# Kernel optimization log

Hardware: AMD Instinct MI355X
Metric: run time of the kernel (lower is better)

The kernel has to match this reference:

```python
import jax, jax.numpy as jnp
import numpy as np

EPS = 1e-5

def cal_pcm(cen, s):
    # circ_shift in the original is exactly a circular roll of the HxW plane.
    r = lambda dy, dx: jnp.roll(cen, (dy, dx), axis=(2, 3))
    s1 = (r(-s, -s) - cen) * (r(s, s) - cen)   # NW/SE diagonal pair
    s2 = (r(-s, 0) - cen) * (r(s, 0) - cen)    # N/S pair
    s3 = (r(-s, s) - cen) * (r(s, -s) - cen)   # NE/SW diagonal pair
    s4 = (r(0, s) - cen) * (r(0, -s) - cen)    # E/W pair
    return jnp.minimum(jnp.minimum(s1, s2), jnp.minimum(s3, s4))

def batchnorm(x, gamma, beta):
    # training-mode BN: batch statistics over (N,H,W)
    mean = x.mean(axis=(0, 2, 3), keepdims=True)
    var = x.var(axis=(0, 2, 3), keepdims=True)
    xn = (x - mean) * jax.lax.rsqrt(var + EPS)
    return xn * gamma[None, :, None, None] + beta[None, :, None, None]

def se_att(x, w1, b1, g1, be1, w2, b2, g2, be2):
    # AdaptiveAvgPool2d(1) -> 1x1 conv -> BN -> ReLU -> 1x1 conv -> BN -> Sigmoid
    p = x.mean(axis=(2, 3), keepdims=True)                      # [B,C,1,1]
    y = jnp.einsum('oc,bcij->boij', w1, p) + b1[None, :, None, None]
    y = jax.nn.relu(batchnorm(y, g1, be1))
    y = jnp.einsum('oc,bcij->boij', w2, y) + b2[None, :, None, None]
    return jax.nn.sigmoid(batchnorm(y, g2, be2))

def setup_inputs() -> dict:
    key = jax.random.key(0)
    ks = jax.random.split(key, 8)
    B, C, H, W = 4, 64, 384, 384
    IC = C // 2
    inp = {
        'cen': jax.random.normal(ks[0], (B, C, H, W), dtype=jnp.float32),
        'bn1_g': jnp.ones((C,), jnp.float32), 'bn1_b': jnp.zeros((C,), jnp.float32),
        'bn2_g': jnp.ones((C,), jnp.float32), 'bn2_b': jnp.zeros((C,), jnp.float32),
        'td_w1': jax.random.normal(ks[1], (IC, C), jnp.float32) * 0.1,
        'td_b1': jnp.zeros((IC,), jnp.float32),
        'td_g1': jnp.ones((IC,), jnp.float32), 'td_be1': jnp.zeros((IC,), jnp.float32),
        'td_w2': jax.random.normal(ks[2], (C, IC), jnp.float32) * 0.1,
        'td_b2': jnp.zeros((C,), jnp.float32),
        'td_g2': jnp.ones((C,), jnp.float32), 'td_be2': jnp.zeros((C,), jnp.float32),
        'bu_w1': jax.random.normal(ks[3], (IC, C), jnp.float32) * 0.1,
        'bu_b1': jnp.zeros((IC,), jnp.float32),
        'bu_g1': jnp.ones((IC,), jnp.float32), 'bu_be1': jnp.zeros((IC,), jnp.float32),
        'bu_w2': jax.random.normal(ks[4], (C, IC), jnp.float32) * 0.1,
        'bu_b2': jnp.zeros((C,), jnp.float32),
        'bu_g2': jnp.ones((C,), jnp.float32), 'bu_be2': jnp.zeros((C,), jnp.float32),
    }
    return inp

def reference(cen, bn1_g, bn1_b, bn2_g, bn2_b,
              td_w1, td_b1, td_g1, td_be1, td_w2, td_b2, td_g2, td_be2,
              bu_w1, bu_b1, bu_g1, bu_be1, bu_w2, bu_b2, bu_g2, bu_be2):
    pcm13 = batchnorm(cal_pcm(cen, 13), bn1_g, bn1_b)
    pcm17 = batchnorm(cal_pcm(cen, 17), bn2_g, bn2_b)
    topdown_wei = se_att(pcm17, td_w1, td_b1, td_g1, td_be1, td_w2, td_b2, td_g2, td_be2)
    bottomup_wei = se_att(pcm13, bu_w1, bu_b1, bu_g1, bu_be1, bu_w2, bu_b2, bu_g2, bu_be2)
    return topdown_wei * pcm13 + bottomup_wei * pcm17
```

## Files before the change

### kernel.cpp

```cpp
#include <hip/hip_runtime.h>
#include <hip/hip_fp16.h>
#include <math.h>

#define HH 384
#define WW 384
#define CNUM 64
#define BNUM 4
#define HWSZ (HH*WW)
#define NPLANES (BNUM*CNUM)
#define EPSBN 1e-5f

#define ROWS_K1 32
#define BPP_K1 (HH/ROWS_K1)
#define NB_K1 (NPLANES*BPP_K1)
#define ROWS_FB 16
#define BPP_FB (HH/ROWS_FB)
#define NB_FB (NPLANES*BPP_FB)

typedef float f4v __attribute__((ext_vector_type(4)));
typedef unsigned int u4v __attribute__((ext_vector_type(4)));

__device__ __forceinline__ void pcm_loads(const float* __restrict__ pp, int h, int w,
      int wp13, int wm13, int wp17, int wm17, float* v)
{
  int hp13 = h+13; if (hp13 >= HH) hp13 -= HH;
  int hm13 = h-13; if (hm13 <  0 ) hm13 += HH;
  int hp17 = h+17; if (hp17 >= HH) hp17 -= HH;
  int hm17 = h-17; if (hm17 <  0 ) hm17 += HH;
  const float* r0   = pp + h*WW;
  const float* rp13 = pp + hp13*WW;
  const float* rm13 = pp + hm13*WW;
  const float* rp17 = pp + hp17*WW;
  const float* rm17 = pp + hm17*WW;
  v[0]  = r0[w];
  v[1]  = rp13[wp13]; v[2]  = rm13[wm13];
  v[3]  = rp13[w];    v[4]  = rm13[w];
  v[5]  = rp13[wm13]; v[6]  = rm13[wp13];
  v[7]  = r0[wm13];   v[8]  = r0[wp13];
  v[9]  = rp17[wp17]; v[10] = rm17[wm17];
  v[11] = rp17[w];    v[12] = rm17[w];
  v[13] = rp17[wm17]; v[14] = rm17[wp17];
  v[15] = r0[wm17];   v[16] = r0[wp17];
}

__device__ __forceinline__ void pcm_eval(const float* v, float& p13, float& p17)
{
  const float d = v[0];
  {
    float s1 = (v[1]-d)*(v[2]-d);
    float s2 = (v[3]-d)*(v[4]-d);
    float s3 = (v[5]-d)*(v[6]-d);
    float s4 = (v[7]-d)*(v[8]-d);
    p13 = fminf(fminf(s1,s2), fminf(s3,s4));
  }
  {
    float s1 = (v[9] -d)*(v[10]-d);
    float s2 = (v[11]-d)*(v[12]-d);
    float s3 = (v[13]-d)*(v[14]-d);
    float s4 = (v[15]-d)*(v[16]-d);
    p17 = fminf(fminf(s1,s2), fminf(s3,s4));
  }
}

template<int NB>
__device__ __forceinline__ int swz_block() {
  return (blockIdx.x & 7)*(NB/8) + (blockIdx.x >> 3);
}

__global__ __launch_bounds__(384) void k1_kernel(const float* __restrict__ cen,
                                                 unsigned int* __restrict__ pcm_ws,
                                                 float* __restrict__ partials)
{
  const int blk = swz_block<NB_K1>();
  const int p   = blk / BPP_K1;
  const int kb  = blk % BPP_K1;
  const int w   = threadIdx.x;
  const float* pp = cen + (size_t)p*HWSZ;
  unsigned int* wp = pcm_ws + (size_t)p*HWSZ;

  int wp13 = w+13; if (wp13 >= WW) wp13 -= WW;
  int wm13 = w-13; if (wm13 <  0 ) wm13 += WW;
  int wp17 = w+17; if (wp17 >= WW) wp17 -= WW;
  int wm17 = w-17; if (wm17 <  0 ) wm17 += WW;

  float s13 = 0.f, q13 = 0.f, s17 = 0.f, q17 = 0.f;
  const int h0 = kb*ROWS_K1;
  for (int r = 0; r < ROWS_K1; r += 2) {
    const int h = h0 + r;
    float va[17], vb[17];
    pcm_loads(pp, h,   w, wp13, wm13, wp17, wm17, va);
    pcm_loads(pp, h+1, w, wp13, wm13, wp17, wm17, vb);
    __builtin_amdgcn_sched_barrier(0);
    float a13, a17, b13, b17;
    pcm_eval(va, a13, a17);
    pcm_eval(vb, b13, b17);
    __half2 ha = __floats2half2_rn(a13, a17);
    __half2 hb = __floats2half2_rn(b13, b17);
    __builtin_nontemporal_store(*reinterpret_cast<unsigned int*>(&ha), &wp[h*WW + w]);
    __builtin_nontemporal_store(*reinterpret_cast<unsigned int*>(&hb), &wp[(h+1)*WW + w]);
    float2 fa = __half22float2(ha);
    float2 fb = __half22float2(hb);
    s13 += fa.x + fb.x; q13 += fa.x*fa.x + fb.x*fb.x;
    s17 += fa.y + fb.y; q17 += fa.y*fa.y + fb.y*fb.y;
  }
  for (int off = 32; off > 0; off >>= 1) {
    s13 += __shfl_down(s13, off);
    q13 += __shfl_down(q13, off);
    s17 += __shfl_down(s17, off);
    q17 += __shfl_down(q17, off);
  }
  __shared__ float red[6][4];
  const int wid = threadIdx.x >> 6;
  if ((threadIdx.x & 63) == 0) {
    red[wid][0] = s13; red[wid][1] = q13; red[wid][2] = s17; red[wid][3] = q17;
  }
  __syncthreads();
  if (threadIdx.x == 0) {
    float a=0.f,b=0.f,c=0.f,d=0.f;
    for (int i = 0; i < 6; ++i) { a+=red[i][0]; b+=red[i][1]; c+=red[i][2]; d+=red[i][3]; }
    float* q = partials + (size_t)blk*4;
    q[0]=a; q[1]=b; q[2]=c; q[3]=d;
  }
}

__device__ void se_mlp(int t, const float* __restrict__ p,
    const float* __restrict__ w1, const float* __restrict__ b1,
    const float* __restrict__ g1, const float* __restrict__ be1,
    const float* __restrict__ w2, const float* __restrict__ b2,
    const float* __restrict__ g2, const float* __restrict__ be2,
    float* y1, float* sc, float* sh, float* wei)
{
  if (t < 128) {
    const int b = t >> 5, o = t & 31;
    float acc = b1[o];
    const float* wr = w1 + o*64;
    const float* pr = p  + b*64;
    #pragma unroll
    for (int c = 0; c < 64; ++c) acc += wr[c]*pr[c];
    y1[t] = acc;
  }
  __syncthreads();
  if (t < 32) {
    float a0=y1[t], a1=y1[32+t], a2=y1[64+t], a3=y1[96+t];
    float m = 0.25f*(a0+a1+a2+a3);
    float q = 0.25f*(a0*a0+a1*a1+a2*a2+a3*a3);
    float v = q - m*m;
    float s = g1[t]*rsqrtf(v + EPSBN);
    sc[t] = s; sh[t] = be1[t] - m*s;
  }
  __syncthreads();
  if (t < 128) {
    const int o = t & 31;
    y1[t] = fmaxf(y1[t]*sc[o] + sh[o], 0.0f);
  }
  __syncthreads();
  {
    const int b = t >> 6, o2 = t & 63;
    float acc = b2[o2];
    const float* wr = w2 + o2*32;
    const float* yr = y1 + b*32;
    #pragma unroll
    for (int o = 0; o < 32; ++o) acc += wr[o]*yr[o];
    wei[t] = acc;
  }
  __syncthreads();
  if (t < 64) {
    float a0=wei[t], a1=wei[64+t], a2=wei[128+t], a3=wei[192+t];
    float m = 0.25f*(a0+a1+a2+a3);
    float q = 0.25f*(a0*a0+a1*a1+a2*a2+a3*a3);
    float v = q - m*m;
    float s = g2[t]*rsqrtf(v + EPSBN);
    sc[t] = s; sh[t] = be2[t] - m*s;
  }
  __syncthreads();
  {
    const int o2 = t & 63;
    float z = wei[t]*sc[o2] + sh[o2];
    wei[t] = 1.0f/(1.0f + expf(-z));
  }
  __syncthreads();
}

__global__ __launch_bounds__(256) void se_kernel(
    const float* __restrict__ partials, int bpp,
    const float* __restrict__ bn1_g, const float* __restrict__ bn1_b,
    const float* __restrict__ bn2_g, const float* __restrict__ bn2_b,
    const float* __restrict__ td_w1, const float* __restrict__ td_b1,
    const float* __restrict__ td_g1, const float* __restrict__ td_be1,
    const float* __restrict__ td_w2, const float* __restrict__ td_b2,
    const float* __restrict__ td_g2, const float* __restrict__ td_be2,
    const float* __restrict__ bu_w1, const float* __restrict__ bu_b1,
    const float* __restrict__ bu_g1, const float* __restrict__ bu_be1,
    const float* __restrict__ bu_w2, const float* __restrict__ bu_b2,
    const float* __restrict__ bu_g2, const float* __restrict__ bu_be2,
    float* __restrict__ coef)
{
  __shared__ float sum13[256], sq13[256], sum17[256], sq17[256];
  __shared__ float scale1[64], shift1[64], scale2[64], shift2[64];
  __shared__ float pm13[256], pm17[256];
  __shared__ float y1[128], sc[64], sh[64];
  __shared__ float tdw[256], buw[256];
  const int t = threadIdx.x;

  {
    float a=0.f,b=0.f,c=0.f,d=0.f;
    for (int kb = 0; kb < bpp; ++kb) {
      const float* q = partials + ((size_t)(t*bpp + kb))*4;
      a += q[0]; b += q[1]; c += q[2]; d += q[3];
    }
    sum13[t]=a; sq13[t]=b; sum17[t]=c; sq17[t]=d;
  }
  __syncthreads();

  if (t < 64) {
    float s=0.f,q=0.f,s2=0.f,q2=0.f;
    for (int b = 0; b < 4; ++b) {
      s  += sum13[b*64+t]; q  += sq13[b*64+t];
      s2 += sum17[b*64+t]; q2 += sq17[b*64+t];
    }
    const float inv = 1.0f/(4.0f*HWSZ);
    float m1 = s*inv,  v1 = q*inv  - m1*m1;
    float c1 = bn1_g[t]*rsqrtf(v1 + EPSBN);
    scale1[t] = c1; shift1[t] = bn1_b[t] - m1*c1;
    float m2 = s2*inv, v2 = q2*inv - m2*m2;
    float c2 = bn2_g[t]*rsqrtf(v2 + EPSBN);
    scale2[t] = c2; shift2[t] = bn2_b[t] - m2*c2;
  }
  __syncthreads();

  {
    const int c = t & 63;
    pm13[t] = (sum13[t]*(1.0f/HWSZ))*scale1[c] + shift1[c];
    pm17[t] = (sum17[t]*(1.0f/HWSZ))*scale2[c] + shift2[c];
  }
  __syncthreads();

  se_mlp(t, pm17, td_w1, td_b1, td_g1, td_be1, td_w2, td_b2, td_g2, td_be2, y1, sc, sh, tdw);
  se_mlp(t, pm13, bu_w1, bu_b1, bu_g1, bu_be1, bu_w2, bu_b2, bu_g2, bu_be2, y1, sc, sh, buw);

  {
    const int c = t & 63;
    float A  = tdw[t]*scale1[c];
    float Bc = buw[t]*scale2[c];
    float Cc = tdw[t]*shift1[c] + buw[t]*shift2[c];
    coef[t*4+0] = A; coef[t*4+1] = Bc; coef[t*4+2] = Cc; coef[t*4+3] = 0.f;
  }
}

#define K3_BLOCKS 4608
#define K3_THREADS 256

__global__ __launch_bounds__(K3_THREADS) void k3_kernel(const u4v* __restrict__ pcm4,
                                                        const f4v* __restrict__ coef4,
                                                        f4v* __restrict__ out4)
{
  const int total = NPLANES*HWSZ/4;
  int i = blockIdx.x*K3_THREADS + threadIdx.x;
  const int stride = K3_BLOCKS*K3_THREADS;
  for (; i < total; i += stride) {
    const int plane = (i*4)/HWSZ;
    const f4v cf = coef4[plane];
    const u4v v = __builtin_nontemporal_load(&pcm4[i]);
    f4v o;
    #pragma unroll
    for (int j = 0; j < 4; ++j) {
      unsigned int u = v[j];
      __half2 hp = *reinterpret_cast<__half2*>(&u);
      float2 f = __half22float2(hp);
      o[j] = cf.x*f.x + cf.y*f.y + cf.z;
    }
    __builtin_nontemporal_store(o, &out4[i]);
  }
}

__global__ __launch_bounds__(384) void passA_kernel(const float* __restrict__ cen,
                                                    float* __restrict__ partials)
{
  const int blk = swz_block<NB_FB>();
  const int p   = blk / BPP_FB;
  const int kb  = blk % BPP_FB;
  const int w   = threadIdx.x;
  const float* pp = cen + (size_t)p*HWSZ;

  int wp13 = w+13; if (wp13 >= WW) wp13 -= WW;
  int wm13 = w-13; if (wm13 <  0 ) wm13 += WW;
  int wp17 = w+17; if (wp17 >= WW) wp17 -= WW;
  int wm17 = w-17; if (wm17 <  0 ) wm17 += WW;

  float s13 = 0.f, q13 = 0.f, s17 = 0.f, q17 = 0.f;
  const int h0 = kb*ROWS_FB;
  for (int r = 0; r < ROWS_FB; r += 2) {
    float va[17], vb[17];
    pcm_loads(pp, h0+r,   w, wp13, wm13, wp17, wm17, va);
    pcm_loads(pp, h0+r+1, w, wp13, wm13, wp17, wm17, vb);
    __builtin_amdgcn_sched_barrier(0);
    float a13, a17, b13, b17;
    pcm_eval(va, a13, a17);
    pcm_eval(vb, b13, b17);
    s13 += a13 + b13; q13 += a13*a13 + b13*b13;
    s17 += a17 + b17; q17 += a17*a17 + b17*b17;
  }
  for (int off = 32; off > 0; off >>= 1) {
    s13 += __shfl_down(s13, off);
    q13 += __shfl_down(q13, off);
    s17 += __shfl_down(s17, off);
    q17 += __shfl_down(q17, off);
  }
  __shared__ float red[6][4];
  const int wid = threadIdx.x >> 6;
  if ((threadIdx.x & 63) == 0) {
    red[wid][0] = s13; red[wid][1] = q13; red[wid][2] = s17; red[wid][3] = q17;
  }
  __syncthreads();
  if (threadIdx.x == 0) {
    float a=0.f,b=0.f,c=0.f,d=0.f;
    for (int i = 0; i < 6; ++i) { a+=red[i][0]; b+=red[i][1]; c+=red[i][2]; d+=red[i][3]; }
    float* q = partials + (size_t)blk*4;
    q[0]=a; q[1]=b; q[2]=c; q[3]=d;
  }
}

__global__ __launch_bounds__(384) void passB_kernel(const float* __restrict__ cen,
                                                    const float* __restrict__ coef,
                                                    float* __restrict__ out)
{
  const int blk = swz_block<NB_FB>();
  const int p   = blk / BPP_FB;
  const int kb  = blk % BPP_FB;
  const int w   = threadIdx.x;
  const float A  = coef[p*4+0];
  const float Bc = coef[p*4+1];
  const float Cc = coef[p*4+2];
  const float* pp = cen + (size_t)p*HWSZ;
  float* op = out + (size_t)p*HWSZ;

  int wp13 = w+13; if (wp13 >= WW) wp13 -= WW;
  int wm13 = w-13; if (wm13 <  0 ) wm13 += WW;
  int wp17 = w+17; if (wp17 >= WW) wp17 -= WW;
  int wm17 = w-17; if (wm17 <  0 ) wm17 += WW;

  const int h0 = kb*ROWS_FB;
  for (int r = 0; r < ROWS_FB; r += 2) {
    const int h = h0 + r;
    float va[17], vb[17];
    pcm_loads(pp, h,   w, wp13, wm13, wp17, wm17, va);
    pcm_loads(pp, h+1, w, wp13, wm13, wp17, wm17, vb);
    __builtin_amdgcn_sched_barrier(0);
    float a13, a17, b13, b17;
    pcm_eval(va, a13, a17);
    pcm_eval(vb, b13, b17);
    __builtin_nontemporal_store(A*a13 + Bc*a17 + Cc, &op[h*WW + w]);
    __builtin_nontemporal_store(A*b13 + Bc*b17 + Cc, &op[(h+1)*WW + w]);
  }
}

extern "C" void kernel_launch(void* const* d_in, const int* in_sizes, int n_in,
                              void* d_out, int out_size, void* d_ws, size_t ws_size,
                              hipStream_t stream) {
  const float* cen = (const float*)d_in[0];
  const size_t PCM_BYTES = (size_t)NPLANES*HWSZ*sizeof(unsigned int);
  const size_t NEED = PCM_BYTES + (size_t)NB_K1*4*sizeof(float) + 256*4*sizeof(float);

  if (ws_size >= NEED) {
    unsigned int* pcm_ws = (unsigned int*)d_ws;
    float* partials = (float*)((char*)d_ws + PCM_BYTES);
    float* coef     = partials + (size_t)NB_K1*4;

    k1_kernel<<<NB_K1, 384, 0, stream>>>(cen, pcm_ws, partials);
    se_kernel<<<1, 256, 0, stream>>>(partials, BPP_K1,
        (const float*)d_in[1],  (const float*)d_in[2],  (const float*)d_in[3],  (const float*)d_in[4],
        (const float*)d_in[5],  (const float*)d_in[6],  (const float*)d_in[7],  (const float*)d_in[8],
        (const float*)d_in[9],  (const float*)d_in[10], (const float*)d_in[11], (const float*)d_in[12],
        (const float*)d_in[13], (const float*)d_in[14], (const float*)d_in[15], (const float*)d_in[16],
        (const float*)d_in[17], (const float*)d_in[18], (const float*)d_in[19], (const float*)d_in[20],
        coef);
    k3_kernel<<<K3_BLOCKS, K3_THREADS, 0, stream>>>((const u4v*)pcm_ws, (const f4v*)coef, (f4v*)d_out);
  } else {
    float* ws = (float*)d_ws;
    float* partials = ws;
    float* coef     = ws + (size_t)NB_FB*4;
    passA_kernel<<<NB_FB, 384, 0, stream>>>(cen, partials);
    se_kernel<<<1, 256, 0, stream>>>(partials, BPP_FB,
        (const float*)d_in[1],  (const float*)d_in[2],  (const float*)d_in[3],  (const float*)d_in[4],
        (const float*)d_in[5],  (const float*)d_in[6],  (const float*)d_in[7],  (const float*)d_in[8],
        (const float*)d_in[9],  (const float*)d_in[10], (const float*)d_in[11], (const float*)d_in[12],
        (const float*)d_in[13], (const float*)d_in[14], (const float*)d_in[15], (const float*)d_in[16],
        (const float*)d_in[17], (const float*)d_in[18], (const float*)d_in[19], (const float*)d_in[20],
        coef);
    passB_kernel<<<NB_FB, 384, 0, stream>>>(cen, coef, (float*)d_out);
  }
}
```

Before: 167.6 us.

## Split BN statistics into separate pass over cached half2 PCM workspace

The stencil kernel no longer computes BN sum/sumsq. It only writes the half2 PCM values, now with ordinary (cacheable) stores instead of nontemporal ones. A new k1b kernel rereads the 151 MB workspace, which it hopes to hit in the MI355X's large last-level cache, and produces per-quarter-plane partials. The change also halves rows per block, drops the sched_barriers, unrolls the loop, and makes the k3 load cacheable. It adds a kernel launch and an extra read of the workspace in exchange for a lighter stencil kernel.

```diff
diff --git a/kernel.cpp b/kernel.cpp
--- a/kernel.cpp
+++ b/kernel.cpp
@@ -10,12 +10,14 @@
 #define NPLANES (BNUM*CNUM)
 #define EPSBN 1e-5f
 
-#define ROWS_K1 32
-#define BPP_K1 (HH/ROWS_K1)
-#define NB_K1 (NPLANES*BPP_K1)
-#define ROWS_FB 16
-#define BPP_FB (HH/ROWS_FB)
-#define NB_FB (NPLANES*BPP_FB)
+#define ROWS_ST 16
+#define BPP_ST (HH/ROWS_ST)
+#define NB_ST (NPLANES*BPP_ST)
+
+#define CHUNKS_PER_PLANE 4
+#define K1B_BLOCKS (NPLANES*CHUNKS_PER_PLANE)
+#define U4_PER_PLANE (HWSZ/4)
+#define U4_PER_CHUNK (U4_PER_PLANE/CHUNKS_PER_PLANE)
 
 typedef float f4v __attribute__((ext_vector_type(4)));
 typedef unsigned int u4v __attribute__((ext_vector_type(4)));
@@ -68,12 +70,11 @@
 }
 
 __global__ __launch_bounds__(384) void k1_kernel(const float* __restrict__ cen,
-                                                 unsigned int* __restrict__ pcm_ws,
-                                                 float* __restrict__ partials)
-{
-  const int blk = swz_block<NB_K1>();
-  const int p   = blk / BPP_K1;
-  const int kb  = blk % BPP_K1;
+                                                 unsigned int* __restrict__ pcm_ws)
+{
+  const int blk = swz_block<NB_ST>();
+  const int p   = blk / BPP_ST;
+  const int kb  = blk % BPP_ST;
   const int w   = threadIdx.x;
   const float* pp = cen + (size_t)p*HWSZ;
   unsigned int* wp = pcm_ws + (size_t)p*HWSZ;
@@ -83,25 +84,41 @@
   int wp17 = w+17; if (wp17 >= WW) wp17 -= WW;
   int wm17 = w-17; if (wm17 <  0 ) wm17 += WW;
 
-  float s13 = 0.f, q13 = 0.f, s17 = 0.f, q17 = 0.f;
-  const int h0 = kb*ROWS_K1;
-  for (int r = 0; r < ROWS_K1; r += 2) {
+  const int h0 = kb*ROWS_ST;
+  #pragma unroll 2
+  for (int r = 0; r < ROWS_ST; r += 2) {
     const int h = h0 + r;
     float va[17], vb[17];
     pcm_loads(pp, h,   w, wp13, wm13, wp17, wm17, va);
     pcm_loads(pp, h+1, w, wp13, wm13, wp17, wm17, vb);
-    __builtin_amdgcn_sched_barrier(0);
     float a13, a17, b13, b17;
     pcm_eval(va, a13, a17);
     pcm_eval(vb, b13, b17);
     __half2 ha = __floats2half2_rn(a13, a17);
     __half2 hb = __floats2half2_rn(b13, b17);
-    __builtin_nontemporal_store(*reinterpret_cast<unsigned int*>(&ha), &wp[h*WW + w]);
-    __builtin_nontemporal_store(*reinterpret_cast<unsigned int*>(&hb), &wp[(h+1)*WW + w]);
-    float2 fa = __half22float2(ha);
-    float2 fb = __half22float2(hb);
-    s13 += fa.x + fb.x; q13 += fa.x*fa.x + fb.x*fb.x;
-    s17 += fa.y + fb.y; q17 += fa.y*fa.y + fb.y*fb.y;
+    wp[h*WW + w]     = *reinterpret_cast<unsigned int*>(&ha);
+    wp[(h+1)*WW + w] = *reinterpret_cast<unsigned int*>(&hb);
+  }
+}
+
+__global__ __launch_bounds__(256) void k1b_kernel(const u4v* __restrict__ pcm4,
+                                                  float* __restrict__ partials)
+{
+  const int b = blockIdx.x;
+  const int plane = b >> 2, q = b & 3;
+  const u4v* base = pcm4 + (size_t)plane*U4_PER_PLANE + (size_t)q*U4_PER_CHUNK;
+
+  float s13 = 0.f, q13 = 0.f, s17 = 0.f, q17 = 0.f;
+  for (int i = threadIdx.x; i < U4_PER_CHUNK; i += 256) {
+    const u4v v = base[i];
+    #pragma unroll
+    for (int j = 0; j < 4; ++j) {
+      unsigned int u = v[j];
+      __half2 hp = *reinterpret_cast<__half2*>(&u);
+      float2 f = __half22float2(hp);
+      s13 += f.x; q13 += f.x*f.x;
+      s17 += f.y; q17 += f.y*f.y;
+    }
   }
   for (int off = 32; off > 0; off >>= 1) {
     s13 += __shfl_down(s13, off);
@@ -109,17 +126,17 @@
     s17 += __shfl_down(s17, off);
     q17 += __shfl_down(q17, off);
   }
-  __shared__ float red[6][4];
+  __shared__ float red[4][4];
   const int wid = threadIdx.x >> 6;
   if ((threadIdx.x & 63) == 0) {
     red[wid][0] = s13; red[wid][1] = q13; red[wid][2] = s17; red[wid][3] = q17;
   }
   __syncthreads();
   if (threadIdx.x == 0) {
-    float a=0.f,b=0.f,c=0.f,d=0.f;
-    for (int i = 0; i < 6; ++i) { a+=red[i][0]; b+=red[i][1]; c+=red[i][2]; d+=red[i][3]; }
-    float* q = partials + (size_t)blk*4;
-    q[0]=a; q[1]=b; q[2]=c; q[3]=d;
+    float a=0.f,bb=0.f,c=0.f,d=0.f;
+    for (int i = 0; i < 4; ++i) { a+=red[i][0]; bb+=red[i][1]; c+=red[i][2]; d+=red[i][3]; }
+    float* out = partials + (size_t)b*4;
+    out[0]=a; out[1]=bb; out[2]=c; out[3]=d;
   }
 }
 
@@ -260,7 +277,7 @@
   for (; i < total; i += stride) {
     const int plane = (i*4)/HWSZ;
     const f4v cf = coef4[plane];
-    const u4v v = __builtin_nontemporal_load(&pcm4[i]);
+    const u4v v = pcm4[i];
     f4v o;
     #pragma unroll
     for (int j = 0; j < 4; ++j) {
@@ -276,9 +293,9 @@
 __global__ __launch_bounds__(384) void passA_kernel(const float* __restrict__ cen,
                                                     float* __restrict__ partials)
 {
-  const int blk = swz_block<NB_FB>();
-  const int p   = blk / BPP_FB;
-  const int kb  = blk % BPP_FB;
+  const int blk = swz_block<NB_ST>();
+  const int p   = blk / BPP_ST;
+  const int kb  = blk % BPP_ST;
   const int w   = threadIdx.x;
   const float* pp = cen + (size_t)p*HWSZ;
 
@@ -288,12 +305,12 @@
   int wm17 = w-17; if (wm17 <  0 ) wm17 += WW;
 
   float s13 = 0.f, q13 = 0.f, s17 = 0.f, q17 = 0.f;
-  const int h0 = kb*ROWS_FB;
-  for (int r = 0; r < ROWS_FB; r += 2) {
+  const int h0 = kb*ROWS_ST;
+  #pragma unroll 2
+  for (int r = 0; r < ROWS_ST; r += 2) {
     float va[17], vb[17];
     pcm_loads(pp, h0+r,   w, wp13, wm13, wp17, wm17, va);
     pcm_loads(pp, h0+r+1, w, wp13, wm13, wp17, wm17, vb);
-    __builtin_amdgcn_sched_barrier(0);
     float a13, a17, b13, b17;
     pcm_eval(va, a13, a17);
     pcm_eval(vb, b13, b17);
@@ -324,9 +341,9 @@
                                                     const float* __restrict__ coef,
                                                     float* __restrict__ out)
 {
-  const int blk = swz_block<NB_FB>();
-  const int p   = blk / BPP_FB;
-  const int kb  = blk % BPP_FB;
+  const int blk = swz_block<NB_ST>();
+  const int p   = blk / BPP_ST;
+  const int kb  = blk % BPP_ST;
   const int w   = threadIdx.x;
   const float A  = coef[p*4+0];
   const float Bc = coef[p*4+1];
@@ -339,13 +356,13 @@
   int wp17 = w+17; if (wp17 >= WW) wp17 -= WW;
   int wm17 = w-17; if (wm17 <  0 ) wm17 += WW;
 
-  const int h0 = kb*ROWS_FB;
-  for (int r = 0; r < ROWS_FB; r += 2) {
+  const int h0 = kb*ROWS_ST;
+  #pragma unroll 2
+  for (int r = 0; r < ROWS_ST; r += 2) {
     const int h = h0 + r;
     float va[17], vb[17];
     pcm_loads(pp, h,   w, wp13, wm13, wp17, wm17, va);
     pcm_loads(pp, h+1, w, wp13, wm13, wp17, wm17, vb);
-    __builtin_amdgcn_sched_barrier(0);
     float a13, a17, b13, b17;
     pcm_eval(va, a13, a17);
     pcm_eval(vb, b13, b17);
@@ -359,15 +376,16 @@
                               hipStream_t stream) {
   const float* cen = (const float*)d_in[0];
   const size_t PCM_BYTES = (size_t)NPLANES*HWSZ*sizeof(unsigned int);
-  const size_t NEED = PCM_BYTES + (size_t)NB_K1*4*sizeof(float) + 256*4*sizeof(float);
+  const size_t NEED = PCM_BYTES + (size_t)K1B_BLOCKS*4*sizeof(float) + 256*4*sizeof(float);
 
   if (ws_size >= NEED) {
     unsigned int* pcm_ws = (unsigned int*)d_ws;
     float* partials = (float*)((char*)d_ws + PCM_BYTES);
-    float* coef     = partials + (size_t)NB_K1*4;
-
-    k1_kernel<<<NB_K1, 384, 0, stream>>>(cen, pcm_ws, partials);
-    se_kernel<<<1, 256, 0, stream>>>(partials, BPP_K1,
+    float* coef     = partials + (size_t)K1B_BLOCKS*4;
+
+    k1_kernel<<<NB_ST, 384, 0, stream>>>(cen, pcm_ws);
+    k1b_kernel<<<K1B_BLOCKS, 256, 0, stream>>>((const u4v*)pcm_ws, partials);
+    se_kernel<<<1, 256, 0, stream>>>(partials, CHUNKS_PER_PLANE,
         (const float*)d_in[1],  (const float*)d_in[2],  (const float*)d_in[3],  (const float*)d_in[4],
         (const float*)d_in[5],  (const float*)d_in[6],  (const float*)d_in[7],  (const float*)d_in[8],
         (const float*)d_in[9],  (const float*)d_in[10], (const float*)d_in[11], (const float*)d_in[12],
@@ -378,15 +396,15 @@
   } else {
     float* ws = (float*)d_ws;
     float* partials = ws;
-    float* coef     = ws + (size_t)NB_FB*4;
-    passA_kernel<<<NB_FB, 384, 0, stream>>>(cen, partials);
-    se_kernel<<<1, 256, 0, stream>>>(partials, BPP_FB,
+    float* coef     = ws + (size_t)NB_ST*4;
+    passA_kernel<<<NB_ST, 384, 0, stream>>>(cen, partials);
+    se_kernel<<<1, 256, 0, stream>>>(partials, BPP_ST,
         (const float*)d_in[1],  (const float*)d_in[2],  (const float*)d_in[3],  (const float*)d_in[4],
         (const float*)d_in[5],  (const float*)d_in[6],  (const float*)d_in[7],  (const float*)d_in[8],
         (const float*)d_in[9],  (const float*)d_in[10], (const float*)d_in[11], (const float*)d_in[12],
         (const float*)d_in[13], (const float*)d_in[14], (const float*)d_in[15], (const float*)d_in[16],
         (const float*)d_in[17], (const float*)d_in[18], (const float*)d_in[19], (const float*)d_in[20],
         coef);
-    passB_kernel<<<NB_FB, 384, 0, stream>>>(cen, coef, (float*)d_out);
-  }
-}
+    passB_kernel<<<NB_ST, 384, 0, stream>>>(cen, coef, (float*)d_out);
+  }
+}
```

Measured after the change: 233.6 us. 1.39x slower.
